# Kernel optimization log

Measured on AMD Instinct MI355X. Metric: run time of the kernel, lower is better.

Reference implementation:

```python
import jax, jax.numpy as jnp
import numpy as np

N_NODES = 10000
N_EDGES = 160000
F = 128
NRB = 32


def setup_inputs() -> dict:
    key = jax.random.key(0)
    ks = jax.random.split(key, 20)
    inp = {
        "s": jax.random.normal(ks[0], (N_NODES, F), jnp.float32),
        "v": jax.random.normal(ks[1], (N_NODES, 3, F), jnp.float32),
        "radial_embeddings_1": jax.random.normal(ks[2], (N_EDGES, NRB), jnp.float32),
        "radial_embeddings_2": jax.random.normal(ks[3], (N_EDGES, NRB), jnp.float32),
        "radial_embeddings_3": jax.random.normal(ks[4], (N_EDGES, NRB), jnp.float32),
        "f_cut_1": jax.random.uniform(ks[5], (N_EDGES,), jnp.float32),
        "f_cut_2": jax.random.uniform(ks[6], (N_EDGES,), jnp.float32),
        "f_cut_3": jax.random.uniform(ks[7], (N_EDGES,), jnp.float32),
        "unit_vectors_1": jax.random.normal(ks[8], (N_EDGES, 3), jnp.float32),
        "unit_vectors_2": jax.random.normal(ks[9], (N_EDGES, 3), jnp.float32),
        "unit_vectors_3": jax.random.normal(ks[10], (N_EDGES, 3), jnp.float32),
        "edge_index": jax.random.randint(ks[11], (2, N_EDGES), 0, N_NODES, jnp.int64),
    }
    # parameters (Linear uses y = x @ W.T + b; we store transposed for x @ W)
    sc1 = 1.0 / np.sqrt(F)
    sc2 = 1.0 / np.sqrt(NRB)
    inp["W1"] = jax.random.uniform(ks[12], (F, F), jnp.float32, -sc1, sc1)
    inp["b1"] = jax.random.uniform(ks[13], (F,), jnp.float32, -sc1, sc1)
    inp["W2"] = jax.random.uniform(ks[14], (F, 8 * F), jnp.float32, -sc1, sc1)
    inp["b2"] = jax.random.uniform(ks[15], (8 * F,), jnp.float32, -sc1, sc1)
    inp["Wr"] = jax.random.uniform(ks[16], (NRB, 8 * F), jnp.float32, -sc2, sc2)
    inp["br"] = jax.random.uniform(ks[17], (8 * F,), jnp.float32, -sc2, sc2)
    return inp


def reference(s, v, radial_embeddings_1, radial_embeddings_2, radial_embeddings_3,
              f_cut_1, f_cut_2, f_cut_3,
              unit_vectors_1, unit_vectors_2, unit_vectors_3,
              edge_index, W1, b1, W2, b2, Wr, br):
    idx_i, idx_j = edge_index[0], edge_index[1]
    n_nodes = s.shape[0]
    nf = W1.shape[0]

    # phi = Linear(F,F) -> SiLU -> Linear(F,8F)   [N, 8F]
    phi = jax.nn.silu(s @ W1 + b1) @ W2 + b2

    # shared-weight radial filter over 3 branches  [E, 8F]
    W = ((radial_embeddings_1 @ Wr + br) * f_cut_1[:, None]
         + (radial_embeddings_2 @ Wr + br) * f_cut_2[:, None]
         + (radial_embeddings_3 @ Wr + br) * f_cut_3[:, None])

    x = phi[idx_j] * W                                    # [E, 8F]
    x_s, x_vv, x_vs1, x_vs2, x_vs3, x_vc1, x_vc2, x_vc3 = jnp.split(x, 8, axis=-1)

    ds = jax.ops.segment_sum(x_s, idx_i, num_segments=n_nodes)

    vj = v[idx_j]                                         # [E, 3, F]
    ex = lambda a: a[:, None, :]                          # [E,1,F] broadcast over xyz
    cr = lambda u: jnp.cross(vj, u[..., None], axis=1)    # [E, 3, F]

    x_v = (vj * ex(x_vv)
           + ex(x_vs1) * unit_vectors_1[..., None]
           + ex(x_vs2) * unit_vectors_2[..., None]
           + ex(x_vs3) * unit_vectors_3[..., None]
           + ex(x_vc1) * cr(unit_vectors_1)
           + ex(x_vc2) * cr(unit_vectors_2)
           + ex(x_vc3) * cr(unit_vectors_3))              # [E, 3, F]

    dv = jax.ops.segment_sum(x_v, idx_i, num_segments=n_nodes)
    return (s + ds, v + dv)
```

## Files before the change

kernel.cpp:

```cpp
#include <hip/hip_runtime.h>

#define N_NODES 10000
#define N_EDGES 160000
#define MAXT     19400
#define NSLOT    (MAXT * 16 + 16)
#define MSG_GRID 5000
#define PHI_BLOCKS 628
#define RC_BLOCKS 5000
#define PAD_BLOCKS 625

typedef __attribute__((ext_vector_type(8))) __bf16 bf16x8;
typedef __attribute__((ext_vector_type(8))) unsigned short u16x8;
typedef __attribute__((ext_vector_type(4))) float f32x4;

static __device__ __forceinline__ unsigned short f2bf(float x) {
    union { float f; unsigned u; } un;
    un.f = x;
    unsigned r = un.u + 0x7fffu + ((un.u >> 16) & 1u);
    return (unsigned short)(r >> 16);
}

static __device__ __forceinline__ float bf2f(unsigned short h) {
    union { unsigned u; float f; } un;
    un.u = ((unsigned)h) << 16;
    return un.f;
}

__global__ __launch_bounds__(256) void init_kernel(
    const float* __restrict__ s, const float* __restrict__ v,
    const int* __restrict__ eix,
    const float* __restrict__ W1, const float* __restrict__ W2,
    const float* __restrict__ Wr,
    float* __restrict__ out0, float* __restrict__ out1,
    unsigned short* __restrict__ vbf2, int* __restrict__ cnt,
    unsigned short* __restrict__ W1T, unsigned short* __restrict__ W2T,
    unsigned short* __restrict__ WrT)
{
    int tid = blockIdx.x * 256 + threadIdx.x;
    if (tid < N_NODES * 96)
        reinterpret_cast<float4*>(out1)[tid] = reinterpret_cast<const float4*>(v)[tid];
    if (tid < N_NODES * 32)
        reinterpret_cast<float4*>(out0)[tid] = reinterpret_cast<const float4*>(s)[tid];
    if (tid < N_NODES * 128) {
        int n = tid >> 7, f = tid & 127;
        ushort4 q;
        q.x = f2bf(v[(size_t)n * 384 + f]);
        q.y = f2bf(v[(size_t)n * 384 + 128 + f]);
        q.z = f2bf(v[(size_t)n * 384 + 256 + f]);
        q.w = 0;
        *reinterpret_cast<ushort4*>(vbf2 + (size_t)tid * 4) = q;
    }
    if (tid < 131072) {
        int n = tid >> 7, k = tid & 127;
        W2T[tid] = f2bf(W2[k * 1024 + n]);
    }
    if (tid < 16384) {
        int n = tid >> 7, k = tid & 127;
        W1T[tid] = f2bf(W1[k * 128 + n]);
    }
    if (tid < 32768) {
        int n = tid >> 5, k = tid & 31;
        WrT[tid] = f2bf(Wr[k * 1024 + n]);
    }
    if (tid < N_EDGES) atomicAdd(&cnt[eix[tid]], 1);
}

__global__ __launch_bounds__(1024) void scan_kernel(
    const int* __restrict__ cnt, int* __restrict__ cursor,
    int* __restrict__ nb, int* __restrict__ tile_node,
    int* __restrict__ ntiles)
{
    __shared__ int ws[16];
    __shared__ int run_s;
    int t = threadIdx.x, lane = t & 63, wid = t >> 6;
    if (t == 0) run_s = 0;
    __syncthreads();
    for (int base = 0; base < N_NODES; base += 1024) {
        int idx = base + t;
        int deg = (idx < N_NODES) ? cnt[idx] : 0;
        int tc = (deg + 15) >> 4;
        int x = tc;
        #pragma unroll
        for (int o = 1; o < 64; o <<= 1) {
            int y = __shfl_up(x, o);
            if (lane >= o) x += y;
        }
        if (lane == 63) ws[wid] = x;
        __syncthreads();
        if (wid == 0) {
            int wv = (lane < 16) ? ws[lane] : 0;
            #pragma unroll
            for (int o = 1; o < 16; o <<= 1) {
                int y = __shfl_up(wv, o);
                if (lane >= o) wv += y;
            }
            if (lane < 16) ws[lane] = wv;
        }
        __syncthreads();
        int wb = wid ? ws[wid - 1] : 0;
        int ex = run_s + wb + x - tc;
        if (idx < N_NODES) {
            nb[idx] = ex * 16;
            cursor[idx] = ex * 16;
            for (int k = 0; k < tc; ++k) tile_node[ex + k] = idx;
        }
        __syncthreads();
        if (t == 0) run_s += ws[15];
        __syncthreads();
    }
    if (t == 0) *ntiles = run_s;
}

__global__ __launch_bounds__(256) void rc_phi_kernel(
    const float* __restrict__ R1, const float* __restrict__ R2,
    const float* __restrict__ R3,
    const float* __restrict__ f1, const float* __restrict__ f2,
    const float* __restrict__ f3,
    const float* __restrict__ u1, const float* __restrict__ u2,
    const float* __restrict__ u3,
    const int* __restrict__ eix, const int* __restrict__ cnt,
    const int* __restrict__ nb, int* __restrict__ cursor,
    unsigned short* __restrict__ Rc_s, float* __restrict__ hdr,
    const float* __restrict__ s, const unsigned short* __restrict__ W1T,
    const float* __restrict__ b1, const unsigned short* __restrict__ W2T,
    const float* __restrict__ b2, unsigned short* __restrict__ phi2)
{
    __shared__ unsigned short h_lds[64][136];
    int bx = blockIdx.x;

    if (bx < PHI_BLOCKS) {
        int t = threadIdx.x, lane = t & 63, w = t >> 6;
        int quad = lane >> 4, l16 = lane & 15;
        int m0 = (bx >> 2) * 64;
        int colg = bx & 3;

        int arow = m0 + w * 16 + l16;
        if (arow > N_NODES - 1) arow = N_NODES - 1;
        bf16x8 afr[4];
        #pragma unroll
        for (int ks = 0; ks < 4; ++ks) {
            const float* sp = s + (size_t)arow * 128 + ks * 32 + quad * 8;
            #pragma unroll
            for (int jj = 0; jj < 8; ++jj) afr[ks][jj] = (__bf16)sp[jj];
        }
        #pragma unroll
        for (int cg = 0; cg < 8; ++cg) {
            int col = cg * 16 + l16;
            f32x4 acc = {0.f, 0.f, 0.f, 0.f};
            #pragma unroll
            for (int ks = 0; ks < 4; ++ks) {
                bf16x8 bf = *reinterpret_cast<const bf16x8*>(W1T + (size_t)col * 128 + ks * 32 + quad * 8);
                acc = __builtin_amdgcn_mfma_f32_16x16x32_bf16(afr[ks], bf, acc, 0, 0, 0);
            }
            float bb = b1[col];
            #pragma unroll
            for (int r = 0; r < 4; ++r) {
                int row = w * 16 + quad * 4 + r;
                float val = acc[r] + bb;
                h_lds[row][col] = f2bf(val / (1.f + __expf(-val)));
            }
        }
        __syncthreads();

        bf16x8 a2[4][4];
        #pragma unroll
        for (int rg = 0; rg < 4; ++rg)
            #pragma unroll
            for (int ks = 0; ks < 4; ++ks)
                a2[rg][ks] = *reinterpret_cast<const bf16x8*>(&h_lds[rg * 16 + l16][ks * 32 + quad * 8]);
        #pragma unroll
        for (int i = 0; i < 4; ++i) {
            int col = colg * 256 + w * 64 + i * 16 + l16;
            f32x4 acc2[4] = {{0,0,0,0},{0,0,0,0},{0,0,0,0},{0,0,0,0}};
            #pragma unroll
            for (int ks = 0; ks < 4; ++ks) {
                bf16x8 bf = *reinterpret_cast<const bf16x8*>(W2T + (size_t)col * 128 + ks * 32 + quad * 8);
                #pragma unroll
                for (int rg = 0; rg < 4; ++rg)
                    acc2[rg] = __builtin_amdgcn_mfma_f32_16x16x32_bf16(a2[rg][ks], bf, acc2[rg], 0, 0, 0);
            }
            float bb = b2[col];
            int f = col & 127, cc = col >> 7;
            #pragma unroll
            for (int rg = 0; rg < 4; ++rg)
                #pragma unroll
                for (int r = 0; r < 4; ++r) {
                    int row = m0 + rg * 16 + quad * 4 + r;
                    if (row < N_NODES)
                        phi2[(size_t)row * 1024 + f * 8 + cc] = f2bf(acc2[rg][r] + bb);
                }
        }
        return;
    }

    bx -= PHI_BLOCKS;
    if (bx >= RC_BLOCKS) {
        int t2 = (bx - RC_BLOCKS) * 256 + threadIdx.x;
        int n = t2 >> 4, r = t2 & 15;
        int deg = cnt[n], tc = (deg + 15) >> 4;
        int p = deg + r;
        if (p < tc * 16) {
            size_t slot = (size_t)nb[n] + p;
            f32x4 z = {0.f, 0.f, 0.f, 0.f};
            f32x4* hp = reinterpret_cast<f32x4*>(hdr + slot * 16);
            hp[0] = z; hp[1] = z; hp[2] = z; hp[3] = z;
            f32x4* rp = reinterpret_cast<f32x4*>(Rc_s + slot * 32);
            rp[0] = z; rp[1] = z; rp[2] = z; rp[3] = z;
        }
        return;
    }

    int tid = bx * 256 + threadIdx.x;
    int e = tid >> 3, sub = tid & 7;
    int lane = threadIdx.x & 63;
    float a = f1[e], b = f2[e], c = f3[e];
    int k0 = sub * 4;
    float4 r1 = *reinterpret_cast<const float4*>(R1 + (size_t)e * 32 + k0);
    float4 r2 = *reinterpret_cast<const float4*>(R2 + (size_t)e * 32 + k0);
    float4 r3 = *reinterpret_cast<const float4*>(R3 + (size_t)e * 32 + k0);
    ushort4 o;
    o.x = f2bf(r1.x * a + r2.x * b + r3.x * c);
    o.y = f2bf(r1.y * a + r2.y * b + r3.y * c);
    o.z = f2bf(r1.z * a + r2.z * b + r3.z * c);
    o.w = f2bf(r1.w * a + r2.w * b + r3.w * c);
    int slot = 0;
    if (sub == 0) slot = atomicAdd(&cursor[eix[e]], 1);
    slot = __shfl(slot, lane & 56);
    *reinterpret_cast<ushort4*>(Rc_s + (size_t)slot * 32 + k0) = o;
    if (sub == 0) {
        float4 h;
        h.x = __int_as_float(eix[N_EDGES + e]);
        h.y = a + b + c;
        h.z = 0.f; h.w = 0.f;
        *reinterpret_cast<float4*>(hdr + (size_t)slot * 16) = h;
    } else if (sub < 4) {
        const float* up = (sub == 1 ? u1 : (sub == 2 ? u2 : u3)) + (size_t)e * 3;
        float4 h;
        h.x = up[0]; h.y = up[1]; h.z = up[2]; h.w = 0.f;
        *reinterpret_cast<float4*>(hdr + (size_t)slot * 16 + (size_t)sub * 4) = h;
    }
}

__global__ __launch_bounds__(512) void msg_kernel(
    const unsigned short* __restrict__ Rc_s, const float* __restrict__ hdr,
    const unsigned short* __restrict__ phi2, const unsigned short* __restrict__ vbf2,
    const unsigned short* __restrict__ WrT, const float* __restrict__ br,
    const int* __restrict__ tile_node, const int* __restrict__ ntiles,
    float* __restrict__ out0, float* __restrict__ out1)
{
    int t = threadIdx.x, lane = t & 63, w = t >> 6;
    int quad = lane >> 4, l16 = lane & 15;
    int fcol = w * 16 + l16;
    const int nt = *ntiles;

    bf16x8 bfrag[8];
    float brv[8];
    #pragma unroll
    for (int c = 0; c < 8; ++c) {
        int col = c * 128 + fcol;
        bfrag[c] = *reinterpret_cast<const bf16x8*>(WrT + (size_t)col * 32 + quad * 8);
        brv[c] = br[col];
    }

    __shared__ float srow[2][16][17];

    int tile = blockIdx.x;
    bf16x8 af;
    if (tile < nt) {
        if (t < 256) srow[0][t >> 4][t & 15] = hdr[(size_t)tile * 256 + t];
        af = *reinterpret_cast<const bf16x8*>(Rc_s + ((size_t)tile * 16 + l16) * 32 + quad * 8);
    }

    for (int k = 0; tile < nt; ++k, tile += MSG_GRID) {
        int p = k & 1;
        __syncthreads();

        f32x4 acc[8];
        #pragma unroll
        for (int c = 0; c < 8; ++c) {
            f32x4 z = {0.f, 0.f, 0.f, 0.f};
            acc[c] = __builtin_amdgcn_mfma_f32_16x16x32_bf16(af, bfrag[c], z, 0, 0, 0);
        }

        int tn = tile + MSG_GRID;
        if (tn < nt) {
            if (t < 256) srow[p ^ 1][t >> 4][t & 15] = hdr[(size_t)tn * 256 + t];
            af = *reinterpret_cast<const bf16x8*>(Rc_s + ((size_t)tn * 16 + l16) * 32 + quad * 8);
        }

        float ds = 0.f, d0 = 0.f, d1 = 0.f, d2 = 0.f;
        #pragma unroll
        for (int r = 0; r < 4; ++r) {
            int row = quad * 4 + r;
            int j = __float_as_int(srow[p][row][0]);
            float fs = srow[p][row][1];
            size_t o = (size_t)j * 128 + fcol;
            u16x8 ph = *reinterpret_cast<const u16x8*>(phi2 + o * 8);
            ushort4 vb = *reinterpret_cast<const ushort4*>(vbf2 + o * 4);
            float x[8];
            #pragma unroll
            for (int c = 0; c < 8; ++c)
                x[c] = bf2f(ph[c]) * (acc[c][r] + brv[c] * fs);
            float vjx = bf2f(vb.x), vjy = bf2f(vb.y), vjz = bf2f(vb.z);
            float u1x = srow[p][row][4],  u1y = srow[p][row][5],  u1z = srow[p][row][6];
            float u2x = srow[p][row][8],  u2y = srow[p][row][9],  u2z = srow[p][row][10];
            float u3x = srow[p][row][12], u3y = srow[p][row][13], u3z = srow[p][row][14];

            ds += x[0];
            d0 += vjx * x[1] + u1x * x[2] + u2x * x[3] + u3x * x[4]
                + x[5] * (vjy * u1z - vjz * u1y)
                + x[6] * (vjy * u2z - vjz * u2y)
                + x[7] * (vjy * u3z - vjz * u3y);
            d1 += vjy * x[1] + u1y * x[2] + u2y * x[3] + u3y * x[4]
                + x[5] * (vjz * u1x - vjx * u1z)
                + x[6] * (vjz * u2x - vjx * u2z)
                + x[7] * (vjz * u3x - vjx * u3z);
            d2 += vjz * x[1] + u1z * x[2] + u2z * x[3] + u3z * x[4]
                + x[5] * (vjx * u1y - vjy * u1x)
                + x[6] * (vjx * u2y - vjy * u2x)
                + x[7] * (vjx * u3y - vjy * u3x);
        }

        ds += __shfl_xor(ds, 16); ds += __shfl_xor(ds, 32);
        d0 += __shfl_xor(d0, 16); d0 += __shfl_xor(d0, 32);
        d1 += __shfl_xor(d1, 16); d1 += __shfl_xor(d1, 32);
        d2 += __shfl_xor(d2, 16); d2 += __shfl_xor(d2, 32);

        if (quad == 0) {
            int node = tile_node[tile];
            atomicAdd(&out0[(size_t)node * 128 + fcol], ds);
            size_t vo = (size_t)node * 384 + fcol;
            atomicAdd(&out1[vo], d0);
            atomicAdd(&out1[vo + 128], d1);
            atomicAdd(&out1[vo + 256], d2);
        }
    }
}

extern "C" void kernel_launch(void* const* d_in, const int* in_sizes, int n_in,
                              void* d_out, int out_size, void* d_ws, size_t ws_size,
                              hipStream_t stream) {
    const float* s  = (const float*)d_in[0];
    const float* v  = (const float*)d_in[1];
    const float* R1 = (const float*)d_in[2];
    const float* R2 = (const float*)d_in[3];
    const float* R3 = (const float*)d_in[4];
    const float* f1 = (const float*)d_in[5];
    const float* f2 = (const float*)d_in[6];
    const float* f3 = (const float*)d_in[7];
    const float* u1 = (const float*)d_in[8];
    const float* u2 = (const float*)d_in[9];
    const float* u3 = (const float*)d_in[10];
    const int*  eix = (const int*)d_in[11];
    const float* W1 = (const float*)d_in[12];
    const float* b1 = (const float*)d_in[13];
    const float* W2 = (const float*)d_in[14];
    const float* b2 = (const float*)d_in[15];
    const float* Wr = (const float*)d_in[16];
    const float* br = (const float*)d_in[17];

    char* ws = (char*)d_ws;
    size_t off = 0;
    auto alloc = [&](size_t bytes) -> void* {
        void* p = ws + off;
        off = (off + bytes + 255) & ~(size_t)255;
        return p;
    };
    int* cnt       = (int*)alloc((size_t)N_NODES * 4);
    int* cursor    = (int*)alloc((size_t)N_NODES * 4);
    int* nb        = (int*)alloc((size_t)N_NODES * 4);
    int* tile_node = (int*)alloc((size_t)MAXT * 4);
    int* ntiles    = (int*)alloc(4);
    unsigned short* Rc_s = (unsigned short*)alloc((size_t)NSLOT * 32 * 2);
    float* hdr           = (float*)alloc((size_t)NSLOT * 16 * 4);
    unsigned short* vbf2 = (unsigned short*)alloc((size_t)N_NODES * 128 * 4 * 2);
    unsigned short* phi2 = (unsigned short*)alloc((size_t)N_NODES * 1024 * 2);
    unsigned short* W1T  = (unsigned short*)alloc(128 * 128 * 2);
    unsigned short* W2T  = (unsigned short*)alloc(1024 * 128 * 2);
    unsigned short* WrT  = (unsigned short*)alloc(1024 * 32 * 2);
    (void)ws_size; (void)in_sizes; (void)n_in; (void)out_size;

    float* out0 = (float*)d_out;
    float* out1 = out0 + (size_t)N_NODES * 128;

    hipMemsetAsync(cnt, 0, (size_t)N_NODES * 4, stream);
    init_kernel<<<5000, 256, 0, stream>>>(s, v, eix, W1, W2, Wr,
                                          out0, out1, vbf2, cnt, W1T, W2T, WrT);
    scan_kernel<<<1, 1024, 0, stream>>>(cnt, cursor, nb, tile_node, ntiles);
    rc_phi_kernel<<<PHI_BLOCKS + RC_BLOCKS + PAD_BLOCKS, 256, 0, stream>>>(
        R1, R2, R3, f1, f2, f3, u1, u2, u3, eix, cnt, nb, cursor, Rc_s, hdr,
        s, W1T, b1, W2T, b2, phi2);
    msg_kernel<<<MSG_GRID, 512, 0, stream>>>(Rc_s, hdr, phi2, vbf2, WrT, br,
                                             tile_node, ntiles, out0, out1);
}
```

Measured before the change: 321.8 us.

## Overlap scan with phi MLP and interleave per-edge records into one buffer

The serial single-block scan now runs as one extra block of the phi MLP kernel, so the degree prefix sum overlaps the node MLP instead of running alone. The scan itself changes to a per-thread sequential pass over 40 nodes each with a 256-thread scan. The separate Rc and header arrays are merged into one 128-byte record per edge slot, so the message kernel reads one contiguous record per edge. LDS reads of the header become vectorized float4 loads. The edge-record kernel is now launched separately after the scan-plus-phi kernel.

```diff
diff --git a/kernel.cpp b/kernel.cpp
--- a/kernel.cpp
+++ b/kernel.cpp
@@ -65,53 +65,122 @@
     if (tid < N_EDGES) atomicAdd(&cnt[eix[tid]], 1);
 }
 
-__global__ __launch_bounds__(1024) void scan_kernel(
+__global__ __launch_bounds__(256) void scan_phi_kernel(
     const int* __restrict__ cnt, int* __restrict__ cursor,
     int* __restrict__ nb, int* __restrict__ tile_node,
-    int* __restrict__ ntiles)
+    int* __restrict__ ntiles,
+    const float* __restrict__ s, const unsigned short* __restrict__ W1T,
+    const float* __restrict__ b1, const unsigned short* __restrict__ W2T,
+    const float* __restrict__ b2, unsigned short* __restrict__ phi2)
 {
-    __shared__ int ws[16];
-    __shared__ int run_s;
-    int t = threadIdx.x, lane = t & 63, wid = t >> 6;
-    if (t == 0) run_s = 0;
-    __syncthreads();
-    for (int base = 0; base < N_NODES; base += 1024) {
-        int idx = base + t;
-        int deg = (idx < N_NODES) ? cnt[idx] : 0;
-        int tc = (deg + 15) >> 4;
-        int x = tc;
+    __shared__ unsigned short h_lds[64][136];
+    __shared__ int ws4[4];
+    int bx = blockIdx.x;
+    int t = threadIdx.x, lane = t & 63, w = t >> 6;
+
+    if (bx == PHI_BLOCKS) {
+        int n0 = t * 40;
+        int sum = 0;
+        for (int i = 0; i < 40; ++i) {
+            int n = n0 + i;
+            if (n < N_NODES) sum += (cnt[n] + 15) >> 4;
+        }
+        int x = sum;
         #pragma unroll
         for (int o = 1; o < 64; o <<= 1) {
             int y = __shfl_up(x, o);
             if (lane >= o) x += y;
         }
-        if (lane == 63) ws[wid] = x;
+        if (lane == 63) ws4[w] = x;
         __syncthreads();
-        if (wid == 0) {
-            int wv = (lane < 16) ? ws[lane] : 0;
-            #pragma unroll
-            for (int o = 1; o < 16; o <<= 1) {
-                int y = __shfl_up(wv, o);
-                if (lane >= o) wv += y;
+        if (t < 4) {
+            int v = ws4[t];
+            #pragma unroll
+            for (int o = 1; o < 4; o <<= 1) {
+                int y = __shfl_up(v, o);
+                if (lane >= o) v += y;
             }
-            if (lane < 16) ws[lane] = wv;
+            ws4[t] = v;
         }
         __syncthreads();
-        int wb = wid ? ws[wid - 1] : 0;
-        int ex = run_s + wb + x - tc;
-        if (idx < N_NODES) {
-            nb[idx] = ex * 16;
-            cursor[idx] = ex * 16;
-            for (int k = 0; k < tc; ++k) tile_node[ex + k] = idx;
-        }
-        __syncthreads();
-        if (t == 0) run_s += ws[15];
-        __syncthreads();
-    }
-    if (t == 0) *ntiles = run_s;
-}
-
-__global__ __launch_bounds__(256) void rc_phi_kernel(
+        int wb = w ? ws4[w - 1] : 0;
+        int run = wb + x - sum;
+        for (int i = 0; i < 40; ++i) {
+            int n = n0 + i;
+            if (n >= N_NODES) break;
+            int tc = (cnt[n] + 15) >> 4;
+            nb[n] = run * 16;
+            cursor[n] = run * 16;
+            for (int k = 0; k < tc; ++k) tile_node[run + k] = n;
+            run += tc;
+        }
+        if (t == 255) *ntiles = run;
+        return;
+    }
+
+    int quad = lane >> 4, l16 = lane & 15;
+    int m0 = (bx >> 2) * 64;
+    int colg = bx & 3;
+
+    int arow = m0 + w * 16 + l16;
+    if (arow > N_NODES - 1) arow = N_NODES - 1;
+    bf16x8 afr[4];
+    #pragma unroll
+    for (int ks = 0; ks < 4; ++ks) {
+        const float* sp = s + (size_t)arow * 128 + ks * 32 + quad * 8;
+        #pragma unroll
+        for (int jj = 0; jj < 8; ++jj) afr[ks][jj] = (__bf16)sp[jj];
+    }
+    #pragma unroll
+    for (int cg = 0; cg < 8; ++cg) {
+        int col = cg * 16 + l16;
+        f32x4 acc = {0.f, 0.f, 0.f, 0.f};
+        #pragma unroll
+        for (int ks = 0; ks < 4; ++ks) {
+            bf16x8 bf = *reinterpret_cast<const bf16x8*>(W1T + (size_t)col * 128 + ks * 32 + quad * 8);
+            acc = __builtin_amdgcn_mfma_f32_16x16x32_bf16(afr[ks], bf, acc, 0, 0, 0);
+        }
+        float bb = b1[col];
+        #pragma unroll
+        for (int r = 0; r < 4; ++r) {
+            int row = w * 16 + quad * 4 + r;
+            float val = acc[r] + bb;
+            h_lds[row][col] = f2bf(val / (1.f + __expf(-val)));
+        }
+    }
+    __syncthreads();
+
+    bf16x8 a2[4][4];
+    #pragma unroll
+    for (int rg = 0; rg < 4; ++rg)
+        #pragma unroll
+        for (int ks = 0; ks < 4; ++ks)
+            a2[rg][ks] = *reinterpret_cast<const bf16x8*>(&h_lds[rg * 16 + l16][ks * 32 + quad * 8]);
+    #pragma unroll
+    for (int i = 0; i < 4; ++i) {
+        int col = colg * 256 + w * 64 + i * 16 + l16;
+        f32x4 acc2[4] = {{0,0,0,0},{0,0,0,0},{0,0,0,0},{0,0,0,0}};
+        #pragma unroll
+        for (int ks = 0; ks < 4; ++ks) {
+            bf16x8 bf = *reinterpret_cast<const bf16x8*>(W2T + (size_t)col * 128 + ks * 32 + quad * 8);
+            #pragma unroll
+            for (int rg = 0; rg < 4; ++rg)
+                acc2[rg] = __builtin_amdgcn_mfma_f32_16x16x32_bf16(a2[rg][ks], bf, acc2[rg], 0, 0, 0);
+        }
+        float bb = b2[col];
+        int f = col & 127, cc = col >> 7;
+        #pragma unroll
+        for (int rg = 0; rg < 4; ++rg)
+            #pragma unroll
+            for (int r = 0; r < 4; ++r) {
+                int row = m0 + rg * 16 + quad * 4 + r;
+                if (row < N_NODES)
+                    phi2[(size_t)row * 1024 + f * 8 + cc] = f2bf(acc2[rg][r] + bb);
+            }
+    }
+}
+
+__global__ __launch_bounds__(256) void rc_pad_kernel(
     const float* __restrict__ R1, const float* __restrict__ R2,
     const float* __restrict__ R3,
     const float* __restrict__ f1, const float* __restrict__ f2,
@@ -120,80 +189,9 @@
     const float* __restrict__ u3,
     const int* __restrict__ eix, const int* __restrict__ cnt,
     const int* __restrict__ nb, int* __restrict__ cursor,
-    unsigned short* __restrict__ Rc_s, float* __restrict__ hdr,
-    const float* __restrict__ s, const unsigned short* __restrict__ W1T,
-    const float* __restrict__ b1, const unsigned short* __restrict__ W2T,
-    const float* __restrict__ b2, unsigned short* __restrict__ phi2)
+    char* __restrict__ rec)
 {
-    __shared__ unsigned short h_lds[64][136];
     int bx = blockIdx.x;
-
-    if (bx < PHI_BLOCKS) {
-        int t = threadIdx.x, lane = t & 63, w = t >> 6;
-        int quad = lane >> 4, l16 = lane & 15;
-        int m0 = (bx >> 2) * 64;
-        int colg = bx & 3;
-
-        int arow = m0 + w * 16 + l16;
-        if (arow > N_NODES - 1) arow = N_NODES - 1;
-        bf16x8 afr[4];
-        #pragma unroll
-        for (int ks = 0; ks < 4; ++ks) {
-            const float* sp = s + (size_t)arow * 128 + ks * 32 + quad * 8;
-            #pragma unroll
-            for (int jj = 0; jj < 8; ++jj) afr[ks][jj] = (__bf16)sp[jj];
-        }
-        #pragma unroll
-        for (int cg = 0; cg < 8; ++cg) {
-            int col = cg * 16 + l16;
-            f32x4 acc = {0.f, 0.f, 0.f, 0.f};
-            #pragma unroll
-            for (int ks = 0; ks < 4; ++ks) {
-                bf16x8 bf = *reinterpret_cast<const bf16x8*>(W1T + (size_t)col * 128 + ks * 32 + quad * 8);
-                acc = __builtin_amdgcn_mfma_f32_16x16x32_bf16(afr[ks], bf, acc, 0, 0, 0);
-            }
-            float bb = b1[col];
-            #pragma unroll
-            for (int r = 0; r < 4; ++r) {
-                int row = w * 16 + quad * 4 + r;
-                float val = acc[r] + bb;
-                h_lds[row][col] = f2bf(val / (1.f + __expf(-val)));
-            }
-        }
-        __syncthreads();
-
-        bf16x8 a2[4][4];
-        #pragma unroll
-        for (int rg = 0; rg < 4; ++rg)
-            #pragma unroll
-            for (int ks = 0; ks < 4; ++ks)
-                a2[rg][ks] = *reinterpret_cast<const bf16x8*>(&h_lds[rg * 16 + l16][ks * 32 + quad * 8]);
-        #pragma unroll
-        for (int i = 0; i < 4; ++i) {
-            int col = colg * 256 + w * 64 + i * 16 + l16;
-            f32x4 acc2[4] = {{0,0,0,0},{0,0,0,0},{0,0,0,0},{0,0,0,0}};
-            #pragma unroll
-            for (int ks = 0; ks < 4; ++ks) {
-                bf16x8 bf = *reinterpret_cast<const bf16x8*>(W2T + (size_t)col * 128 + ks * 32 + quad * 8);
-                #pragma unroll
-                for (int rg = 0; rg < 4; ++rg)
-                    acc2[rg] = __builtin_amdgcn_mfma_f32_16x16x32_bf16(a2[rg][ks], bf, acc2[rg], 0, 0, 0);
-            }
-            float bb = b2[col];
-            int f = col & 127, cc = col >> 7;
-            #pragma unroll
-            for (int rg = 0; rg < 4; ++rg)
-                #pragma unroll
-                for (int r = 0; r < 4; ++r) {
-                    int row = m0 + rg * 16 + quad * 4 + r;
-                    if (row < N_NODES)
-                        phi2[(size_t)row * 1024 + f * 8 + cc] = f2bf(acc2[rg][r] + bb);
-                }
-        }
-        return;
-    }
-
-    bx -= PHI_BLOCKS;
     if (bx >= RC_BLOCKS) {
         int t2 = (bx - RC_BLOCKS) * 256 + threadIdx.x;
         int n = t2 >> 4, r = t2 & 15;
@@ -202,10 +200,9 @@
         if (p < tc * 16) {
             size_t slot = (size_t)nb[n] + p;
             f32x4 z = {0.f, 0.f, 0.f, 0.f};
-            f32x4* hp = reinterpret_cast<f32x4*>(hdr + slot * 16);
-            hp[0] = z; hp[1] = z; hp[2] = z; hp[3] = z;
-            f32x4* rp = reinterpret_cast<f32x4*>(Rc_s + slot * 32);
-            rp[0] = z; rp[1] = z; rp[2] = z; rp[3] = z;
+            f32x4* rp = reinterpret_cast<f32x4*>(rec + slot * 128);
+            #pragma unroll
+            for (int q = 0; q < 8; ++q) rp[q] = z;
         }
         return;
     }
@@ -226,23 +223,24 @@
     int slot = 0;
     if (sub == 0) slot = atomicAdd(&cursor[eix[e]], 1);
     slot = __shfl(slot, lane & 56);
-    *reinterpret_cast<ushort4*>(Rc_s + (size_t)slot * 32 + k0) = o;
+    *reinterpret_cast<ushort4*>(rec + (size_t)slot * 128 + k0 * 2) = o;
+    float* hf = reinterpret_cast<float*>(rec + (size_t)slot * 128 + 64);
     if (sub == 0) {
         float4 h;
         h.x = __int_as_float(eix[N_EDGES + e]);
         h.y = a + b + c;
         h.z = 0.f; h.w = 0.f;
-        *reinterpret_cast<float4*>(hdr + (size_t)slot * 16) = h;
+        *reinterpret_cast<float4*>(hf) = h;
     } else if (sub < 4) {
         const float* up = (sub == 1 ? u1 : (sub == 2 ? u2 : u3)) + (size_t)e * 3;
         float4 h;
         h.x = up[0]; h.y = up[1]; h.z = up[2]; h.w = 0.f;
-        *reinterpret_cast<float4*>(hdr + (size_t)slot * 16 + (size_t)sub * 4) = h;
+        *reinterpret_cast<float4*>(hf + sub * 4) = h;
     }
 }
 
 __global__ __launch_bounds__(512) void msg_kernel(
-    const unsigned short* __restrict__ Rc_s, const float* __restrict__ hdr,
+    const char* __restrict__ rec,
     const unsigned short* __restrict__ phi2, const unsigned short* __restrict__ vbf2,
     const unsigned short* __restrict__ WrT, const float* __restrict__ br,
     const int* __restrict__ tile_node, const int* __restrict__ ntiles,
@@ -252,6 +250,7 @@
     int quad = lane >> 4, l16 = lane & 15;
     int fcol = w * 16 + l16;
     const int nt = *ntiles;
+    const float* recf = reinterpret_cast<const float*>(rec);
 
     bf16x8 bfrag[8];
     float brv[8];
@@ -262,13 +261,14 @@
         brv[c] = br[col];
     }
 
-    __shared__ float srow[2][16][17];
+    __shared__ __align__(16) float srow[2][16][20];
 
     int tile = blockIdx.x;
     bf16x8 af;
     if (tile < nt) {
-        if (t < 256) srow[0][t >> 4][t & 15] = hdr[(size_t)tile * 256 + t];
-        af = *reinterpret_cast<const bf16x8*>(Rc_s + ((size_t)tile * 16 + l16) * 32 + quad * 8);
+        if (t < 256)
+            srow[0][t >> 4][t & 15] = recf[((size_t)tile * 16 + (t >> 4)) * 32 + 16 + (t & 15)];
+        af = *reinterpret_cast<const bf16x8*>(rec + ((size_t)tile * 16 + l16) * 128 + quad * 16);
     }
 
     for (int k = 0; tile < nt; ++k, tile += MSG_GRID) {
@@ -284,16 +284,21 @@
 
         int tn = tile + MSG_GRID;
         if (tn < nt) {
-            if (t < 256) srow[p ^ 1][t >> 4][t & 15] = hdr[(size_t)tn * 256 + t];
-            af = *reinterpret_cast<const bf16x8*>(Rc_s + ((size_t)tn * 16 + l16) * 32 + quad * 8);
+            if (t < 256)
+                srow[p ^ 1][t >> 4][t & 15] = recf[((size_t)tn * 16 + (t >> 4)) * 32 + 16 + (t & 15)];
+            af = *reinterpret_cast<const bf16x8*>(rec + ((size_t)tn * 16 + l16) * 128 + quad * 16);
         }
 
         float ds = 0.f, d0 = 0.f, d1 = 0.f, d2 = 0.f;
         #pragma unroll
         for (int r = 0; r < 4; ++r) {
-            int row = quad * 4 + r;
-            int j = __float_as_int(srow[p][row][0]);
-            float fs = srow[p][row][1];
+            const float* rw = srow[p][quad * 4 + r];
+            float2 jf = *reinterpret_cast<const float2*>(rw);
+            f32x4 U1 = *reinterpret_cast<const f32x4*>(rw + 4);
+            f32x4 U2 = *reinterpret_cast<const f32x4*>(rw + 8);
+            f32x4 U3 = *reinterpret_cast<const f32x4*>(rw + 12);
+            int j = __float_as_int(jf.x);
+            float fs = jf.y;
             size_t o = (size_t)j * 128 + fcol;
             u16x8 ph = *reinterpret_cast<const u16x8*>(phi2 + o * 8);
             ushort4 vb = *reinterpret_cast<const ushort4*>(vbf2 + o * 4);
@@ -302,23 +307,20 @@
             for (int c = 0; c < 8; ++c)
                 x[c] = bf2f(ph[c]) * (acc[c][r] + brv[c] * fs);
             float vjx = bf2f(vb.x), vjy = bf2f(vb.y), vjz = bf2f(vb.z);
-            float u1x = srow[p][row][4],  u1y = srow[p][row][5],  u1z = srow[p][row][6];
-            float u2x = srow[p][row][8],  u2y = srow[p][row][9],  u2z = srow[p][row][10];
-            float u3x = srow[p][row][12], u3y = srow[p][row][13], u3z = srow[p][row][14];
 
             ds += x[0];
-            d0 += vjx * x[1] + u1x * x[2] + u2x * x[3] + u3x * x[4]
-                + x[5] * (vjy * u1z - vjz * u1y)
-                + x[6] * (vjy * u2z - vjz * u2y)
-                + x[7] * (vjy * u3z - vjz * u3y);
-            d1 += vjy * x[1] + u1y * x[2] + u2y * x[3] + u3y * x[4]
-                + x[5] * (vjz * u1x - vjx * u1z)
-                + x[6] * (vjz * u2x - vjx * u2z)
-                + x[7] * (vjz * u3x - vjx * u3z);
-            d2 += vjz * x[1] + u1z * x[2] + u2z * x[3] + u3z * x[4]
-                + x[5] * (vjx * u1y - vjy * u1x)
-                + x[6] * (vjx * u2y - vjy * u2x)
-                + x[7] * (vjx * u3y - vjy * u3x);
+            d0 += vjx * x[1] + U1.x * x[2] + U2.x * x[3] + U3.x * x[4]
+                + x[5] * (vjy * U1.z - vjz * U1.y)
+                + x[6] * (vjy * U2.z - vjz * U2.y)
+                + x[7] * (vjy * U3.z - vjz * U3.y);
+            d1 += vjy * x[1] + U1.y * x[2] + U2.y * x[3] + U3.y * x[4]
+                + x[5] * (vjz * U1.x - vjx * U1.z)
+                + x[6] * (vjz * U2.x - vjx * U2.z)
+                + x[7] * (vjz * U3.x - vjx * U3.z);
+            d2 += vjz * x[1] + U1.z * x[2] + U2.z * x[3] + U3.z * x[4]
+                + x[5] * (vjx * U1.y - vjy * U1.x)
+                + x[6] * (vjx * U2.y - vjy * U2.x)
+                + x[7] * (vjx * U3.y - vjy * U3.x);
         }
 
         ds += __shfl_xor(ds, 16); ds += __shfl_xor(ds, 32);
@@ -371,8 +373,7 @@
     int* nb        = (int*)alloc((size_t)N_NODES * 4);
     int* tile_node = (int*)alloc((size_t)MAXT * 4);
     int* ntiles    = (int*)alloc(4);
-    unsigned short* Rc_s = (unsigned short*)alloc((size_t)NSLOT * 32 * 2);
-    float* hdr           = (float*)alloc((size_t)NSLOT * 16 * 4);
+    char* rec            = (char*)alloc((size_t)NSLOT * 128);
     unsigned short* vbf2 = (unsigned short*)alloc((size_t)N_NODES * 128 * 4 * 2);
     unsigned short* phi2 = (unsigned short*)alloc((size_t)N_NODES * 1024 * 2);
     unsigned short* W1T  = (unsigned short*)alloc(128 * 128 * 2);
@@ -386,10 +387,10 @@
     hipMemsetAsync(cnt, 0, (size_t)N_NODES * 4, stream);
     init_kernel<<<5000, 256, 0, stream>>>(s, v, eix, W1, W2, Wr,
                                           out0, out1, vbf2, cnt, W1T, W2T, WrT);
-    scan_kernel<<<1, 1024, 0, stream>>>(cnt, cursor, nb, tile_node, ntiles);
-    rc_phi_kernel<<<PHI_BLOCKS + RC_BLOCKS + PAD_BLOCKS, 256, 0, stream>>>(
-        R1, R2, R3, f1, f2, f3, u1, u2, u3, eix, cnt, nb, cursor, Rc_s, hdr,
-        s, W1T, b1, W2T, b2, phi2);
-    msg_kernel<<<MSG_GRID, 512, 0, stream>>>(Rc_s, hdr, phi2, vbf2, WrT, br,
+    scan_phi_kernel<<<PHI_BLOCKS + 1, 256, 0, stream>>>(
+        cnt, cursor, nb, tile_node, ntiles, s, W1T, b1, W2T, b2, phi2);
+    rc_pad_kernel<<<RC_BLOCKS + PAD_BLOCKS, 256, 0, stream>>>(
+        R1, R2, R3, f1, f2, f3, u1, u2, u3, eix, cnt, nb, cursor, rec);
+    msg_kernel<<<MSG_GRID, 512, 0, stream>>>(rec, phi2, vbf2, WrT, br,
                                              tile_node, ntiles, out0, out1);
 }
```

New measurement: 320.0 us. No clear change (-0.6%).
